# Optimization experiments

Hardware: AMD Instinct MI355X
Metric: run time of the kernel (lower is better)

## Reference

```python
import jax, jax.numpy as jnp
import numpy as np

N_HEADS = 16

def setup_inputs() -> dict:
    key = jax.random.key(0)
    ks = jax.random.split(key, 5)
    C = 1024
    B, T = 2, 2048
    s_in = 1.0 / np.sqrt(C)
    x = jax.random.normal(ks[0], (B, T, C), dtype=jnp.float32)
    W_qkv = jax.random.normal(ks[1], (C, 3 * C), dtype=jnp.float32) * s_in
    b_qkv = jnp.zeros((3 * C,), dtype=jnp.float32)
    W_proj = jax.random.normal(ks[2], (C, C), dtype=jnp.float32) * s_in
    b_proj = jnp.zeros((C,), dtype=jnp.float32)
    return {"x": x, "W_qkv": W_qkv, "b_qkv": b_qkv, "W_proj": W_proj, "b_proj": b_proj}

def reference(x, W_qkv, b_qkv, W_proj, b_proj):
    B, T, C = x.shape
    H = N_HEADS
    D = C // H  # head dim
    qkv = x @ W_qkv + b_qkv                      # [B,T,3C]
    q, k, v = jnp.split(qkv, 3, axis=-1)
    # [B,T,C] -> [B,H,T,D]
    q = q.reshape(B, T, H, D).transpose(0, 2, 1, 3)
    k = k.reshape(B, T, H, D).transpose(0, 2, 1, 3)
    v = v.reshape(B, T, H, D).transpose(0, 2, 1, 3)
    scale = 1.0 / np.sqrt(D)
    att = jnp.einsum('bhqd,bhkd->bhqk', q, k) * scale  # [B,H,T,T]
    causal = jnp.tril(jnp.ones((T, T), dtype=bool))
    att = jnp.where(causal[None, None], att, -jnp.inf)
    att = jax.nn.softmax(att, axis=-1)
    y = jnp.einsum('bhqk,bhkd->bhqd', att, v)    # [B,H,T,D]
    y = y.transpose(0, 2, 1, 3).reshape(B, T, C)
    return y @ W_proj + b_proj
```

## Files before the change

kernel.cpp:

```cpp
#include <hip/hip_runtime.h>
#include <hip/hip_bf16.h>
#include <stdint.h>

#define DEVI __device__ __forceinline__

typedef __attribute__((ext_vector_type(8))) short bf16x8;
typedef __attribute__((ext_vector_type(4))) float f32x4;
typedef __attribute__((ext_vector_type(4))) short short4v;
typedef __attribute__((ext_vector_type(4))) float float4v;
typedef __attribute__((ext_vector_type(2))) unsigned int uint2v;

#define QSCALE 0.1803368801111204f

DEVI unsigned short f2bf(float f) {
  union { float f; unsigned u; } v; v.f = f;
  unsigned r = v.u + 0x7FFFu + ((v.u >> 16) & 1u);
  return (unsigned short)(r >> 16);
}

DEVI float bf2f(unsigned short u) {
  union { unsigned u; float f; } v; v.u = ((unsigned)u) << 16; return v.f;
}

DEVI unsigned cvt_pk_bf16(float lo, float hi) {
  unsigned r;
  asm("v_cvt_pk_bf16_f32 %0, %1, %2" : "=v"(r) : "v"(lo), "v"(hi));
  return r;
}

DEVI void async16(unsigned short* lds, const unsigned short* g) {
  __builtin_amdgcn_global_load_lds(
      (const __attribute__((address_space(1))) void*)g,
      (__attribute__((address_space(3))) void*)lds, 16, 0, 0);
}

DEVI int xcd_swz_flat() {
  int orig = (int)blockIdx.x + (int)gridDim.x * (int)blockIdx.y;
  int cpx = ((int)gridDim.x * (int)gridDim.y) >> 3;
  return (orig & 7) * cpx + (orig >> 3);
}

__device__ const signed char TTX[8][3] = {
  {15,15, 0},{ 7,13, 1},{14,12, 2},{14,10, 3},
  {13,10, 8},{ 6, 9, 9},{12,11, 8},{11, 5, 4}};
__device__ const signed char TTS[8][3] = {
  {0,1,2},{2,0,2},{0,0,2},{1,0,2},{1,1,0},{2,0,1},{1,0,1},{1,2,2}};

__global__ void k_prep(const float* __restrict__ x, unsigned short* __restrict__ xb,
                       const float* __restrict__ Wq, const float* __restrict__ Wp,
                       unsigned short* __restrict__ WqT, unsigned short* __restrict__ WpT) {
  __shared__ float tile[32][33];
  const int id = (int)blockIdx.x;
  if (id < 4096) {
    int i = id * 256 + (int)threadIdx.x;
    float4v f = *reinterpret_cast<const float4v*>(x + (size_t)i * 4);
    short4v o;
#pragma unroll
    for (int j = 0; j < 4; ++j) o[j] = (short)f2bf(f[j]);
    *reinterpret_cast<short4v*>(xb + (size_t)i * 4) = o;
    return;
  }
  const int flat = id - 4096;
  const int bx = flat & 127, k0 = (flat >> 7) * 32;
  const float* W;
  unsigned short* Wt;
  int N, n0;
  if (bx < 96) { W = Wq; Wt = WqT; N = 3072; n0 = bx * 32; }
  else         { W = Wp; Wt = WpT; N = 1024; n0 = (bx - 96) * 32; }
  const int K = 1024;
  int r = threadIdx.x >> 5, c = threadIdx.x & 31;
#pragma unroll
  for (int i = 0; i < 4; ++i)
    tile[r + i * 8][c] = W[(size_t)(k0 + r + i * 8) * N + n0 + c];
  __syncthreads();
#pragma unroll
  for (int i = 0; i < 4; ++i)
    Wt[(size_t)(n0 + r + i * 8) * K + k0 + c] = f2bf(tile[c][r + i * 8]);
}

DEVI void stage_ab(unsigned short* AsB, unsigned short* BsB,
                   const unsigned short* Ab, const unsigned short* Bb,
                   int K, int k0, int tid) {
  int row = tid >> 2, cc = (tid & 3) * 8;
  async16(&AsB[tid * 8], Ab + (size_t)row * K + k0 + cc);
  async16(&BsB[tid * 8], Bb + (size_t)row * K + k0 + cc);
}

__global__ __launch_bounds__(512)
void k_gemm(const unsigned short* __restrict__ A,
            const unsigned short* __restrict__ Bt,
            const float* __restrict__ bias,
            unsigned short* __restrict__ qkv,
            unsigned short* __restrict__ vt,
            int M, int N, int K) {
  __shared__ __align__(16) unsigned short As[2][128 * 32];
  __shared__ __align__(16) unsigned short Bs[2][128 * 32];
  const int tid = threadIdx.x;
  const int swzf = xcd_swz_flat();
  const int m0 = (swzf / (int)gridDim.x) * 128, n0 = (swzf % (int)gridDim.x) * 128;
  const int lane = tid & 63, w = tid >> 6;
  const int wr = (w >> 2) * 64, wc = (w & 3) * 32;
  const int lr = lane & 15, lg = lane >> 4;
  f32x4 acc[4][2] = {};
  const unsigned short* Ab = A + (size_t)m0 * K;
  const unsigned short* Bb = Bt + (size_t)n0 * K;

  const int ns = K >> 5;
  stage_ab(As[0], Bs[0], Ab, Bb, K, 0, tid);
  stage_ab(As[1], Bs[1], Ab, Bb, K, 32, tid);
  asm volatile("s_waitcnt vmcnt(2)" ::: "memory");
  __builtin_amdgcn_s_barrier();
  __builtin_amdgcn_sched_barrier(0);

  for (int s = 0; s < ns; ++s) {
    const int cur = s & 1;
    bf16x8 af[4], bfr[2];
#pragma unroll
    for (int m = 0; m < 4; ++m)
      af[m] = *reinterpret_cast<const bf16x8*>(&As[cur][(wr + m * 16 + lr) * 32 + lg * 8]);
#pragma unroll
    for (int n = 0; n < 2; ++n)
      bfr[n] = *reinterpret_cast<const bf16x8*>(&Bs[cur][(wc + n * 16 + lr) * 32 + lg * 8]);
#pragma unroll
    for (int m = 0; m < 4; ++m)
#pragma unroll
      for (int n = 0; n < 2; ++n)
        acc[m][n] = __builtin_amdgcn_mfma_f32_16x16x32_bf16(af[m], bfr[n], acc[m][n], 0, 0, 0);
    __builtin_amdgcn_s_barrier();
    const int ks = (s + 2 < ns) ? (s + 2) * 32 : 0;
    stage_ab(As[cur], Bs[cur], Ab, Bb, K, ks, tid);
    asm volatile("s_waitcnt vmcnt(2)" ::: "memory");
    __builtin_amdgcn_s_barrier();
    __builtin_amdgcn_sched_barrier(0);
  }
#pragma unroll
  for (int n = 0; n < 2; ++n) {
    int col = n0 + wc + n * 16 + lr;
    float bv = bias[col];
    int sel = col >> 10, cc = col & 1023;
    int h = cc >> 6, d = cc & 63;
    if (sel < 2) {
      float sc = (sel == 0) ? QSCALE : 1.0f;
#pragma unroll
      for (int m = 0; m < 4; ++m) {
#pragma unroll
        for (int r = 0; r < 4; ++r) {
          int row = m0 + wr + m * 16 + lg * 4 + r;
          int bh = ((row >> 11) << 4) + h;
          int t = row & 2047;
          qkv[((size_t)(sel * 32 + bh) * 2048 + t) * 64 + d] = f2bf((acc[m][n][r] + bv) * sc);
        }
      }
    } else {
#pragma unroll
      for (int m = 0; m < 4; ++m) {
        int row0 = m0 + wr + m * 16 + lg * 4;
        int bh = ((row0 >> 11) << 4) + h;
        int t0 = row0 & 2047;
        short4v pk;
#pragma unroll
        for (int r = 0; r < 4; ++r) pk[r] = (short)f2bf(acc[m][n][r] + bv);
        *reinterpret_cast<short4v*>(&vt[((size_t)(bh * 64 + d)) * 2048 + t0]) = pk;
      }
    }
  }
}

__global__ __launch_bounds__(256)
void k_gemmP(const unsigned short* __restrict__ A,
             const unsigned short* __restrict__ Bt,
             const float* __restrict__ bias,
             float* __restrict__ O, int M, int N, int K) {
  __shared__ __align__(16) unsigned short As[2][64 * 32];
  __shared__ __align__(16) unsigned short Bs[2][64 * 32];
  const int tid = threadIdx.x;
  const int swzf = xcd_swz_flat();
  const int m0 = (swzf / (int)gridDim.x) * 64, n0 = (swzf % (int)gridDim.x) * 64;
  const int lane = tid & 63, w = tid >> 6;
  const int wr = (w >> 1) * 32, wc = (w & 1) * 32;
  const int lr = lane & 15, lg = lane >> 4;
  f32x4 acc[2][2] = {};
  const unsigned short* Ab = A + (size_t)m0 * K;
  const unsigned short* Bb = Bt + (size_t)n0 * K;

  auto stage = [&](unsigned short* AsB, unsigned short* BsB, int k0) {
    int row = tid >> 2, cc = (tid & 3) * 8;
    async16(&AsB[tid * 8], Ab + (size_t)row * K + k0 + cc);
    async16(&BsB[tid * 8], Bb + (size_t)row * K + k0 + cc);
  };

  const int ns = K >> 5;
  stage(As[0], Bs[0], 0);
  stage(As[1], Bs[1], 32);
  asm volatile("s_waitcnt vmcnt(2)" ::: "memory");
  __builtin_amdgcn_s_barrier();
  __builtin_amdgcn_sched_barrier(0);

  for (int s = 0; s < ns; ++s) {
    const int cur = s & 1;
    bf16x8 af[2], bfr[2];
#pragma unroll
    for (int m = 0; m < 2; ++m)
      af[m] = *reinterpret_cast<const bf16x8*>(&As[cur][(wr + m * 16 + lr) * 32 + lg * 8]);
#pragma unroll
    for (int n = 0; n < 2; ++n)
      bfr[n] = *reinterpret_cast<const bf16x8*>(&Bs[cur][(wc + n * 16 + lr) * 32 + lg * 8]);
#pragma unroll
    for (int m = 0; m < 2; ++m)
#pragma unroll
      for (int n = 0; n < 2; ++n)
        acc[m][n] = __builtin_amdgcn_mfma_f32_16x16x32_bf16(af[m], bfr[n], acc[m][n], 0, 0, 0);
    __builtin_amdgcn_s_barrier();
    const int ks = (s + 2 < ns) ? (s + 2) * 32 : 0;
    stage(As[cur], Bs[cur], ks);
    asm volatile("s_waitcnt vmcnt(2)" ::: "memory");
    __builtin_amdgcn_s_barrier();
    __builtin_amdgcn_sched_barrier(0);
  }
#pragma unroll
  for (int n = 0; n < 2; ++n) {
    int col = n0 + wc + n * 16 + lr;
    float bv = bias[col];
#pragma unroll
    for (int m = 0; m < 2; ++m)
#pragma unroll
      for (int r = 0; r < 4; ++r) {
        int row = m0 + wr + m * 16 + lg * 4 + r;
        O[(size_t)row * N + col] = acc[m][n][r] + bv;
      }
  }
}

DEVI void stage_kv(unsigned short* KsB, unsigned short* VsB,
                   const unsigned short* Kbh, const unsigned short* Vbh,
                   int k0, int tid, int srow, int gcol) {
  async16(&KsB[tid * 8], Kbh + (size_t)(k0 + srow) * 64 + gcol);
  async16(&VsB[tid * 8], Vbh + (size_t)srow * 2048 + k0 + gcol);
}

__global__ __launch_bounds__(512)
void k_attn(const unsigned short* __restrict__ Qg,
            const unsigned short* __restrict__ Kg,
            const unsigned short* __restrict__ Vtg,
            unsigned short* __restrict__ Y,
            unsigned short* __restrict__ po,
            float2* __restrict__ pml) {
  __shared__ __align__(16) unsigned short Ks[2][64 * 64];
  __shared__ __align__(16) unsigned short Vs[2][64 * 64];
  __shared__ __align__(16) unsigned short Ps[8][16 * 64];
  const int orig = (int)blockIdx.x;
  const int xcd = orig & 7;
  const int p = orig >> 3;
  const int slot = p >> 5;
  const int q = p & 31;
  const int type = q >> 2, cpy = q & 3;
  const int bh = xcd * 4 + ((cpy + slot) & 3);
  const int x = TTX[type][slot];
  const int sf = TTS[type][slot];
  const int nsplit = (sf == 2) ? 1 : 2;
  const int s = (sf == 2) ? 0 : sf;
  const int tA = (nsplit == 2 && s == 1) ? (x + 1) : 0;
  const int tB = (nsplit == 2 && s == 0) ? (x + 1) : (2 * x + 2);
  const int tid = threadIdx.x, lane = tid & 63, w = tid >> 6;
  const int lr = lane & 15, lg = lane >> 4;
  const int swz = (lane & 7) * 8;
  const int psw = (lr & 7) * 8;
  const unsigned short* Kbh = Kg + (size_t)bh * 2048 * 64;
  const unsigned short* Vbh = Vtg + (size_t)bh * 64 * 2048;

  const int qw = x * 128 + w * 16;
  const unsigned short* Qrow = Qg + ((size_t)bh * 2048 + qw + lr) * 64;
  bf16x8 qa0 = *reinterpret_cast<const bf16x8*>(&Qrow[lg * 8]);
  bf16x8 qa1 = *reinterpret_cast<const bf16x8*>(&Qrow[32 + lg * 8]);

  float l_run = 0.f;
  f32x4 o[4] = {};

  const int srow = tid >> 3;
  const int gcol = ((tid & 7) ^ (srow & 7)) * 8;

  stage_kv(Ks[0], Vs[0], Kbh, Vbh, tA * 64, tid, srow, gcol);
  stage_kv(Ks[1], Vs[1], Kbh, Vbh, (tA + 1) * 64, tid, srow, gcol);
  asm volatile("s_waitcnt vmcnt(2)" ::: "memory");
  __builtin_amdgcn_s_barrier();
  __builtin_amdgcn_sched_barrier(0);

  for (int t = tA; t < tB; ++t) {
    const int cur = (t - tA) & 1;
    const int k0 = t * 64;
    if (k0 <= qw + 15) {
      const unsigned short* KsC = Ks[cur];
      const unsigned short* VsC = Vs[cur];

      f32x4 sc[4];
      __builtin_amdgcn_s_setprio(1);
#pragma unroll
      for (int n = 0; n < 4; ++n) {
        bf16x8 kb0 = *reinterpret_cast<const bf16x8*>(&KsC[(n * 16 + lr) * 64 + ((lg * 8) ^ swz)]);
        bf16x8 kb1 = *reinterpret_cast<const bf16x8*>(&KsC[(n * 16 + lr) * 64 + ((32 + lg * 8) ^ swz)]);
        f32x4 z = {0.f, 0.f, 0.f, 0.f};
        z = __builtin_amdgcn_mfma_f32_16x16x32_bf16(kb0, qa0, z, 0, 0, 0);
        z = __builtin_amdgcn_mfma_f32_16x16x32_bf16(kb1, qa1, z, 0, 0, 0);
        sc[n] = z;
      }
      __builtin_amdgcn_s_setprio(0);
      if (k0 + 63 > qw) {
        const int klim = qw + lr - k0 - lg * 4;
#pragma unroll
        for (int n = 0; n < 4; ++n)
#pragma unroll
          for (int r = 0; r < 4; ++r)
            if (n * 16 + r > klim) sc[n][r] = -1e30f;
      }
#pragma unroll
      for (int n = 0; n < 4; ++n)
#pragma unroll
        for (int r = 0; r < 4; ++r) {
          sc[n][r] = __builtin_exp2f(sc[n][r]);
          l_run += sc[n][r];
        }
#pragma unroll
      for (int n = 0; n < 4; ++n) {
        uint2v pk;
        pk[0] = cvt_pk_bf16(sc[n][0], sc[n][1]);
        pk[1] = cvt_pk_bf16(sc[n][2], sc[n][3]);
        *reinterpret_cast<uint2v*>(&Ps[w][lr * 64 + ((n * 16 + lg * 4) ^ psw)]) = pk;
      }
      __builtin_amdgcn_s_setprio(1);
#pragma unroll
      for (int jj = 0; jj < 2; ++jj) {
        bf16x8 pa = *reinterpret_cast<const bf16x8*>(&Ps[w][lr * 64 + ((jj * 32 + lg * 8) ^ psw)]);
#pragma unroll
        for (int n = 0; n < 4; ++n) {
          bf16x8 vb = *reinterpret_cast<const bf16x8*>(
              &VsC[(n * 16 + lr) * 64 + ((jj * 32 + lg * 8) ^ swz)]);
          o[n] = __builtin_amdgcn_mfma_f32_16x16x32_bf16(pa, vb, o[n], 0, 0, 0);
        }
      }
      __builtin_amdgcn_s_setprio(0);
    }
    __builtin_amdgcn_s_barrier();
    {
      const int ts = (t + 2 < tB) ? (t + 2) : tA;
      stage_kv(Ks[cur], Vs[cur], Kbh, Vbh, ts * 64, tid, srow, gcol);
    }
    asm volatile("s_waitcnt vmcnt(2)" ::: "memory");
    __builtin_amdgcn_s_barrier();
    __builtin_amdgcn_sched_barrier(0);
  }
  l_run += __shfl_xor(l_run, 16, 64);
  l_run += __shfl_xor(l_run, 32, 64);
  const int b = bh >> 4, h = bh & 15;
  if (nsplit == 1) {
    float rl = 1.0f / l_run;
    float rlo[4];
#pragma unroll
    for (int r = 0; r < 4; ++r) rlo[r] = __shfl(rl, lg * 4 + r, 64);
#pragma unroll
    for (int r = 0; r < 4; ++r) {
      int t = qw + lg * 4 + r;
#pragma unroll
      for (int n = 0; n < 4; ++n)
        Y[((size_t)(b * 2048 + t)) * 1024 + h * 64 + n * 16 + lr] = f2bf(o[n][r] * rlo[r]);
    }
  } else {
    const int g = bh * 8 + (x - 8);
    if (lg == 0) {
      float2 v; v.x = 0.f; v.y = l_run;
      pml[(g * 2 + s) * 128 + w * 16 + lr] = v;
    }
    float oo[4][4];
#pragma unroll
    for (int r = 0; r < 4; ++r)
#pragma unroll
      for (int n = 0; n < 4; ++n) oo[r][n] = o[n][r];
    if (s == 0) {
#pragma unroll
      for (int r = 0; r < 4; ++r) {
        int t = qw + lg * 4 + r;
#pragma unroll
        for (int n = 0; n < 4; ++n)
          Y[((size_t)(b * 2048 + t)) * 1024 + h * 64 + n * 16 + lr] = f2bf(oo[r][n]);
      }
    } else {
#pragma unroll
      for (int r = 0; r < 4; ++r) {
        int row = w * 16 + lg * 4 + r;
#pragma unroll
        for (int n = 0; n < 4; ++n)
          po[((size_t)g * 128 + row) * 64 + n * 16 + lr] = f2bf(oo[r][n]);
      }
    }
  }
}

__global__ __launch_bounds__(256)
void k_merge(unsigned short* __restrict__ Y,
             const unsigned short* __restrict__ po,
             const float2* __restrict__ pml) {
  const int g = (int)blockIdx.x;
  const int bh = g >> 3, x = (g & 7) + 8;
  const int b = bh >> 4, h = bh & 15;
  const int row = threadIdx.x >> 1;
  const int d0 = ((int)threadIdx.x & 1) * 32;
  float2 p0 = pml[(g * 2 + 0) * 128 + row];
  float2 p1 = pml[(g * 2 + 1) * 128 + row];
  float m = fmaxf(p0.x, p1.x);
  float a0 = __builtin_exp2f(p0.x - m), a1 = __builtin_exp2f(p1.x - m);
  float inv = 1.0f / (p0.y * a0 + p1.y * a1);
  float c0 = a0 * inv, c1 = a1 * inv;
  size_t yb = ((size_t)(b * 2048 + x * 128 + row)) * 1024 + h * 64 + d0;
  size_t pb = ((size_t)g * 128 + row) * 64 + d0;
#pragma unroll
  for (int i = 0; i < 4; ++i) {
    bf16x8 yv = *reinterpret_cast<const bf16x8*>(&Y[yb + i * 8]);
    bf16x8 pv = *reinterpret_cast<const bf16x8*>(&po[pb + i * 8]);
    bf16x8 ov;
#pragma unroll
    for (int jj = 0; jj < 8; ++jj)
      ov[jj] = (short)f2bf(bf2f((unsigned short)yv[jj]) * c0 +
                           bf2f((unsigned short)pv[jj]) * c1);
    *reinterpret_cast<bf16x8*>(&Y[yb + i * 8]) = ov;
  }
}

extern "C" void kernel_launch(void* const* d_in, const int* in_sizes, int n_in,
                              void* d_out, int out_size, void* d_ws, size_t ws_size,
                              hipStream_t stream) {
  const float* x     = (const float*)d_in[0];
  const float* Wqkv  = (const float*)d_in[1];
  const float* bqkv  = (const float*)d_in[2];
  const float* Wproj = (const float*)d_in[3];
  const float* bproj = (const float*)d_in[4];
  float* out = (float*)d_out;

  uint8_t* ws = (uint8_t*)d_ws;
  unsigned short* xb     = (unsigned short*)(ws);
  unsigned short* wqkvT  = (unsigned short*)(ws + ((size_t)8  << 20));
  unsigned short* wprojT = (unsigned short*)(ws + ((size_t)14 << 20));
  unsigned short* qkvb   = (unsigned short*)(ws + ((size_t)16 << 20));
  unsigned short* vt     = (unsigned short*)(ws + ((size_t)32 << 20));
  unsigned short* po     = (unsigned short*)(ws + ((size_t)8  << 20));
  float2*         pml    = (float2*)(ws + ((size_t)12 << 20));

  k_prep<<<dim3(8192, 1), 256, 0, stream>>>(x, xb, Wqkv, Wproj, wqkvT, wprojT);
  k_gemm<<<dim3(24, 32), 512, 0, stream>>>(xb, wqkvT, bqkv, qkvb, vt, 4096, 3072, 1024);
  k_attn<<<dim3(768, 1), 512, 0, stream>>>(qkvb, qkvb + (size_t)32 * 2048 * 64, vt, xb, po, pml);
  k_merge<<<dim3(256, 1), 256, 0, stream>>>(xb, po, pml);
  k_gemmP<<<dim3(16, 64), 256, 0, stream>>>(xb, wprojT, bproj, out, 4096, 1024, 1024);
}
```

Measured before the change: 103.9 us.

## Process two 16-row query groups per wave in attention, halve block threads

```diff
diff --git a/kernel.cpp b/kernel.cpp
--- a/kernel.cpp
+++ b/kernel.cpp
@@ -233,12 +233,18 @@
 
 DEVI void stage_kv(unsigned short* KsB, unsigned short* VsB,
                    const unsigned short* Kbh, const unsigned short* Vbh,
-                   int k0, int tid, int srow, int gcol) {
-  async16(&KsB[tid * 8], Kbh + (size_t)(k0 + srow) * 64 + gcol);
-  async16(&VsB[tid * 8], Vbh + (size_t)srow * 2048 + k0 + gcol);
-}
-
-__global__ __launch_bounds__(512)
+                   int k0, int tid) {
+#pragma unroll
+  for (int i = 0; i < 2; ++i) {
+    int c = i * 256 + tid;
+    int srow = c >> 3;
+    int gcol = ((c & 7) ^ (srow & 7)) * 8;
+    async16(&KsB[c * 8], Kbh + (size_t)(k0 + srow) * 64 + gcol);
+    async16(&VsB[c * 8], Vbh + (size_t)srow * 2048 + k0 + gcol);
+  }
+}
+
+__global__ __launch_bounds__(256)
 void k_attn(const unsigned short* __restrict__ Qg,
             const unsigned short* __restrict__ Kg,
             const unsigned short* __restrict__ Vtg,
@@ -268,73 +274,105 @@
   const unsigned short* Kbh = Kg + (size_t)bh * 2048 * 64;
   const unsigned short* Vbh = Vtg + (size_t)bh * 64 * 2048;
 
-  const int qw = x * 128 + w * 16;
-  const unsigned short* Qrow = Qg + ((size_t)bh * 2048 + qw + lr) * 64;
-  bf16x8 qa0 = *reinterpret_cast<const bf16x8*>(&Qrow[lg * 8]);
-  bf16x8 qa1 = *reinterpret_cast<const bf16x8*>(&Qrow[32 + lg * 8]);
-
-  float l_run = 0.f;
-  f32x4 o[4] = {};
-
-  const int srow = tid >> 3;
-  const int gcol = ((tid & 7) ^ (srow & 7)) * 8;
-
-  stage_kv(Ks[0], Vs[0], Kbh, Vbh, tA * 64, tid, srow, gcol);
-  stage_kv(Ks[1], Vs[1], Kbh, Vbh, (tA + 1) * 64, tid, srow, gcol);
-  asm volatile("s_waitcnt vmcnt(2)" ::: "memory");
+  const int qw = x * 128 + w * 32;
+  const unsigned short* Qr0 = Qg + ((size_t)bh * 2048 + qw + lr) * 64;
+  const unsigned short* Qr1 = Qg + ((size_t)bh * 2048 + qw + 16 + lr) * 64;
+  bf16x8 qaA0 = *reinterpret_cast<const bf16x8*>(&Qr0[lg * 8]);
+  bf16x8 qaB0 = *reinterpret_cast<const bf16x8*>(&Qr0[32 + lg * 8]);
+  bf16x8 qaA1 = *reinterpret_cast<const bf16x8*>(&Qr1[lg * 8]);
+  bf16x8 qaB1 = *reinterpret_cast<const bf16x8*>(&Qr1[32 + lg * 8]);
+
+  float l0 = 0.f, l1 = 0.f;
+  f32x4 o0[4] = {}, o1[4] = {};
+
+  stage_kv(Ks[0], Vs[0], Kbh, Vbh, tA * 64, tid);
+  stage_kv(Ks[1], Vs[1], Kbh, Vbh, (tA + 1) * 64, tid);
+  asm volatile("s_waitcnt vmcnt(4)" ::: "memory");
   __builtin_amdgcn_s_barrier();
   __builtin_amdgcn_sched_barrier(0);
 
   for (int t = tA; t < tB; ++t) {
     const int cur = (t - tA) & 1;
     const int k0 = t * 64;
-    if (k0 <= qw + 15) {
+    if (k0 <= qw + 31) {
+      const bool g0on = (k0 <= qw + 15);
       const unsigned short* KsC = Ks[cur];
       const unsigned short* VsC = Vs[cur];
 
-      f32x4 sc[4];
+      f32x4 s0[4], s1[4];
       __builtin_amdgcn_s_setprio(1);
 #pragma unroll
       for (int n = 0; n < 4; ++n) {
         bf16x8 kb0 = *reinterpret_cast<const bf16x8*>(&KsC[(n * 16 + lr) * 64 + ((lg * 8) ^ swz)]);
         bf16x8 kb1 = *reinterpret_cast<const bf16x8*>(&KsC[(n * 16 + lr) * 64 + ((32 + lg * 8) ^ swz)]);
-        f32x4 z = {0.f, 0.f, 0.f, 0.f};
-        z = __builtin_amdgcn_mfma_f32_16x16x32_bf16(kb0, qa0, z, 0, 0, 0);
-        z = __builtin_amdgcn_mfma_f32_16x16x32_bf16(kb1, qa1, z, 0, 0, 0);
-        sc[n] = z;
+        if (g0on) {
+          f32x4 z = {0.f, 0.f, 0.f, 0.f};
+          z = __builtin_amdgcn_mfma_f32_16x16x32_bf16(kb0, qaA0, z, 0, 0, 0);
+          z = __builtin_amdgcn_mfma_f32_16x16x32_bf16(kb1, qaB0, z, 0, 0, 0);
+          s0[n] = z;
+        }
+        f32x4 z1 = {0.f, 0.f, 0.f, 0.f};
+        z1 = __builtin_amdgcn_mfma_f32_16x16x32_bf16(kb0, qaA1, z1, 0, 0, 0);
+        z1 = __builtin_amdgcn_mfma_f32_16x16x32_bf16(kb1, qaB1, z1, 0, 0, 0);
+        s1[n] = z1;
       }
       __builtin_amdgcn_s_setprio(0);
-      if (k0 + 63 > qw) {
+      if (g0on && k0 + 63 > qw) {
         const int klim = qw + lr - k0 - lg * 4;
 #pragma unroll
         for (int n = 0; n < 4; ++n)
 #pragma unroll
           for (int r = 0; r < 4; ++r)
-            if (n * 16 + r > klim) sc[n][r] = -1e30f;
-      }
-#pragma unroll
-      for (int n = 0; n < 4; ++n)
+            if (n * 16 + r > klim) s0[n][r] = -1e30f;
+      }
+      if (k0 + 63 > qw + 16) {
+        const int klim = qw + 16 + lr - k0 - lg * 4;
+#pragma unroll
+        for (int n = 0; n < 4; ++n)
+#pragma unroll
+          for (int r = 0; r < 4; ++r)
+            if (n * 16 + r > klim) s1[n][r] = -1e30f;
+      }
+      if (g0on) {
+#pragma unroll
+        for (int n = 0; n < 4; ++n) {
+#pragma unroll
+          for (int r = 0; r < 4; ++r) {
+            s0[n][r] = __builtin_exp2f(s0[n][r]);
+            l0 += s0[n][r];
+          }
+          uint2v pk;
+          pk[0] = cvt_pk_bf16(s0[n][0], s0[n][1]);
+          pk[1] = cvt_pk_bf16(s0[n][2], s0[n][3]);
+          *reinterpret_cast<uint2v*>(&Ps[w * 2][lr * 64 + ((n * 16 + lg * 4) ^ psw)]) = pk;
+        }
+      }
+#pragma unroll
+      for (int n = 0; n < 4; ++n) {
 #pragma unroll
         for (int r = 0; r < 4; ++r) {
-          sc[n][r] = __builtin_exp2f(sc[n][r]);
-          l_run += sc[n][r];
-        }
-#pragma unroll
-      for (int n = 0; n < 4; ++n) {
+          s1[n][r] = __builtin_exp2f(s1[n][r]);
+          l1 += s1[n][r];
+        }
         uint2v pk;
-        pk[0] = cvt_pk_bf16(sc[n][0], sc[n][1]);
-        pk[1] = cvt_pk_bf16(sc[n][2], sc[n][3]);
-        *reinterpret_cast<uint2v*>(&Ps[w][lr * 64 + ((n * 16 + lg * 4) ^ psw)]) = pk;
+        pk[0] = cvt_pk_bf16(s1[n][0], s1[n][1]);
+        pk[1] = cvt_pk_bf16(s1[n][2], s1[n][3]);
+        *reinterpret_cast<uint2v*>(&Ps[w * 2 + 1][lr * 64 + ((n * 16 + lg * 4) ^ psw)]) = pk;
       }
       __builtin_amdgcn_s_setprio(1);
 #pragma unroll
       for (int jj = 0; jj < 2; ++jj) {
-        bf16x8 pa = *reinterpret_cast<const bf16x8*>(&Ps[w][lr * 64 + ((jj * 32 + lg * 8) ^ psw)]);
+        bf16x8 pa0, pa1;
+        if (g0on)
+          pa0 = *reinterpret_cast<const bf16x8*>(&Ps[w * 2][lr * 64 + ((jj * 32 + lg * 8) ^ psw)]);
+        pa1 = *reinterpret_cast<const bf16x8*>(&Ps[w * 2 + 1][lr * 64 + ((jj * 32 + lg * 8) ^ psw)]);
 #pragma unroll
         for (int n = 0; n < 4; ++n) {
           bf16x8 vb = *reinterpret_cast<const bf16x8*>(
               &VsC[(n * 16 + lr) * 64 + ((jj * 32 + lg * 8) ^ swz)]);
-          o[n] = __builtin_amdgcn_mfma_f32_16x16x32_bf16(pa, vb, o[n], 0, 0, 0);
+          if (g0on)
+            o0[n] = __builtin_amdgcn_mfma_f32_16x16x32_bf16(pa0, vb, o0[n], 0, 0, 0);
+          o1[n] = __builtin_amdgcn_mfma_f32_16x16x32_bf16(pa1, vb, o1[n], 0, 0, 0);
         }
       }
       __builtin_amdgcn_s_setprio(0);
@@ -342,53 +380,60 @@
     __builtin_amdgcn_s_barrier();
     {
       const int ts = (t + 2 < tB) ? (t + 2) : tA;
-      stage_kv(Ks[cur], Vs[cur], Kbh, Vbh, ts * 64, tid, srow, gcol);
-    }
-    asm volatile("s_waitcnt vmcnt(2)" ::: "memory");
+      stage_kv(Ks[cur], Vs[cur], Kbh, Vbh, ts * 64, tid);
+    }
+    asm volatile("s_waitcnt vmcnt(4)" ::: "memory");
     __builtin_amdgcn_s_barrier();
     __builtin_amdgcn_sched_barrier(0);
   }
-  l_run += __shfl_xor(l_run, 16, 64);
-  l_run += __shfl_xor(l_run, 32, 64);
+  l0 += __shfl_xor(l0, 16, 64);
+  l0 += __shfl_xor(l0, 32, 64);
+  l1 += __shfl_xor(l1, 16, 64);
+  l1 += __shfl_xor(l1, 32, 64);
   const int b = bh >> 4, h = bh & 15;
   if (nsplit == 1) {
-    float rl = 1.0f / l_run;
-    float rlo[4];
-#pragma unroll
-    for (int r = 0; r < 4; ++r) rlo[r] = __shfl(rl, lg * 4 + r, 64);
-#pragma unroll
-    for (int r = 0; r < 4; ++r) {
-      int t = qw + lg * 4 + r;
-#pragma unroll
-      for (int n = 0; n < 4; ++n)
-        Y[((size_t)(b * 2048 + t)) * 1024 + h * 64 + n * 16 + lr] = f2bf(o[n][r] * rlo[r]);
+#pragma unroll
+    for (int gr = 0; gr < 2; ++gr) {
+      const f32x4* o = gr ? o1 : o0;
+      float rl = 1.0f / (gr ? l1 : l0);
+      float rlo[4];
+#pragma unroll
+      for (int r = 0; r < 4; ++r) rlo[r] = __shfl(rl, lg * 4 + r, 64);
+#pragma unroll
+      for (int r = 0; r < 4; ++r) {
+        int t = qw + gr * 16 + lg * 4 + r;
+#pragma unroll
+        for (int n = 0; n < 4; ++n)
+          Y[((size_t)(b * 2048 + t)) * 1024 + h * 64 + n * 16 + lr] = f2bf(o[n][r] * rlo[r]);
+      }
     }
   } else {
-    const int g = bh * 8 + (x - 8);
+    const int g2 = bh * 8 + (x - 8);
     if (lg == 0) {
-      float2 v; v.x = 0.f; v.y = l_run;
-      pml[(g * 2 + s) * 128 + w * 16 + lr] = v;
-    }
-    float oo[4][4];
-#pragma unroll
-    for (int r = 0; r < 4; ++r)
-#pragma unroll
-      for (int n = 0; n < 4; ++n) oo[r][n] = o[n][r];
-    if (s == 0) {
-#pragma unroll
-      for (int r = 0; r < 4; ++r) {
-        int t = qw + lg * 4 + r;
-#pragma unroll
-        for (int n = 0; n < 4; ++n)
-          Y[((size_t)(b * 2048 + t)) * 1024 + h * 64 + n * 16 + lr] = f2bf(oo[r][n]);
-      }
-    } else {
-#pragma unroll
-      for (int r = 0; r < 4; ++r) {
-        int row = w * 16 + lg * 4 + r;
-#pragma unroll
-        for (int n = 0; n < 4; ++n)
-          po[((size_t)g * 128 + row) * 64 + n * 16 + lr] = f2bf(oo[r][n]);
+      float2 v0; v0.x = 0.f; v0.y = l0;
+      pml[(g2 * 2 + s) * 128 + w * 32 + lr] = v0;
+      float2 v1; v1.x = 0.f; v1.y = l1;
+      pml[(g2 * 2 + s) * 128 + w * 32 + 16 + lr] = v1;
+    }
+#pragma unroll
+    for (int gr = 0; gr < 2; ++gr) {
+      const f32x4* o = gr ? o1 : o0;
+      if (s == 0) {
+#pragma unroll
+        for (int r = 0; r < 4; ++r) {
+          int t = qw + gr * 16 + lg * 4 + r;
+#pragma unroll
+          for (int n = 0; n < 4; ++n)
+            Y[((size_t)(b * 2048 + t)) * 1024 + h * 64 + n * 16 + lr] = f2bf(o[n][r]);
+        }
+      } else {
+#pragma unroll
+        for (int r = 0; r < 4; ++r) {
+          int row = w * 32 + gr * 16 + lg * 4 + r;
+#pragma unroll
+          for (int n = 0; n < 4; ++n)
+            po[((size_t)g2 * 128 + row) * 64 + n * 16 + lr] = f2bf(o[n][r]);
+        }
       }
     }
   }
@@ -445,7 +490,7 @@
 
   k_prep<<<dim3(8192, 1), 256, 0, stream>>>(x, xb, Wqkv, Wproj, wqkvT, wprojT);
   k_gemm<<<dim3(24, 32), 512, 0, stream>>>(xb, wqkvT, bqkv, qkvb, vt, 4096, 3072, 1024);
-  k_attn<<<dim3(768, 1), 512, 0, stream>>>(qkvb, qkvb + (size_t)32 * 2048 * 64, vt, xb, po, pml);
+  k_attn<<<dim3(768, 1), 256, 0, stream>>>(qkvb, qkvb + (size_t)32 * 2048 * 64, vt, xb, po, pml);
   k_merge<<<dim3(256, 1), 256, 0, stream>>>(xb, po, pml);
   k_gemmP<<<dim3(16, 64), 256, 0, stream>>>(xb, wprojT, bproj, out, 4096, 1024, 1024);
 }
```

Measured after the change: 109.1 us. 5.0% more time.
